# Kernel tuning notes

Hardware: AMD Instinct MI355X
Metric: run time of the kernel (lower is better)

## Reference

```python
import jax, jax.numpy as jnp
import numpy as np

H, KV, D, S = 32, 8, 128, 2048
HID = H * D
L = S  # cache length
LAYER_IDX = 0


def rotate_half(x, axis):
    x1, x2 = jnp.split(x, 2, axis=axis)
    return jnp.concatenate([-x2, x1], axis=axis)


def setup_inputs() -> dict:
    key = jax.random.key(0)
    ks = jax.random.split(key, 9)
    scale = 0.02
    hidden_states = jax.random.normal(ks[0], (1, HID, 1, S), jnp.float32)
    wq = jax.random.normal(ks[1], (H * D, HID), jnp.float32) * scale
    wk = jax.random.normal(ks[2], (KV * D, HID), jnp.float32) * scale
    wv = jax.random.normal(ks[3], (KV * D, HID), jnp.float32) * scale
    wo = jax.random.normal(ks[4], (HID, H * D), jnp.float32) * scale
    bq = jax.random.normal(ks[5], (H * D,), jnp.float32) * scale
    bk = jax.random.normal(ks[6], (KV * D,), jnp.float32) * scale
    bv = jax.random.normal(ks[7], (KV * D,), jnp.float32) * scale
    # RoPE tables (rotate-half convention): (1,1,S,D) and transposed (1,1,D,S)
    inv_freq = 1.0 / (10000.0 ** (np.arange(0, D, 2, dtype=np.float32) / D))
    t = np.arange(S, dtype=np.float32)
    freqs = np.outer(t, inv_freq)                    # (S, D/2)
    emb = np.concatenate([freqs, freqs], axis=-1)    # (S, D)
    cos = jnp.asarray(np.cos(emb), jnp.float32)[None, None]
    sin = jnp.asarray(np.sin(emb), jnp.float32)[None, None]
    cos_t = jnp.swapaxes(cos, -1, -2)
    sin_t = jnp.swapaxes(sin, -1, -2)
    # causal mask in transposed (cache_len, q_len) layout: key pos l visible iff l <= s
    lpos = np.arange(L)[:, None]
    spos = np.arange(S)[None, :]
    attention_mask = jnp.asarray(np.where(lpos <= spos, 0.0, -1e9).astype(np.float32))[None, None]
    key_cache = jnp.zeros((1, KV, L, D), jnp.float32)
    value_cache = jnp.zeros((1, KV, L, D), jnp.float32)
    return dict(hidden_states=hidden_states, wq=wq, bq=bq, wk=wk, bk=bk, wv=wv, bv=bv,
                wo=wo, cos=cos, sin=sin, cos_t=cos_t, sin_t=sin_t,
                attention_mask=attention_mask, key_cache=key_cache,
                value_cache=value_cache, cache_position=0)


def reference(hidden_states, wq, bq, wk, bk, wv, bv, wo, cos, sin, cos_t, sin_t,
              attention_mask, key_cache, value_cache, cache_position):
    x = hidden_states[0, :, 0, :]                          # (HID, S) channels-first
    q = wq @ x + bq[:, None]                               # (H*D, S)
    k = wk @ x + bk[:, None]                               # (KV*D, S)
    v = wv @ x + bv[:, None]
    q = q.reshape(H, D, S)                                 # (H, D, S)
    k = jnp.swapaxes(k.reshape(KV, D, S), 1, 2)            # (KV, S, D)
    v = jnp.swapaxes(v.reshape(KV, D, S), 1, 2)            # (KV, S, D)
    # RoPE: Q rotated along D (dim=-2 in NCHW), K along last dim
    q = q * cos_t[0] + rotate_half(q, axis=1) * sin_t[0]
    k = k * cos[0] + rotate_half(k, axis=2) * sin[0]
    # KV-cache in-place update at cache_position
    kc = jax.lax.dynamic_update_slice(key_cache, k[None], (LAYER_IDX, 0, cache_position, 0))
    vc = jax.lax.dynamic_update_slice(value_cache, v[None], (LAYER_IDX, 0, cache_position, 0))
    kk = kc[LAYER_IDX]                                     # (KV, L, D)
    vv = vc[LAYER_IDX]                                     # (KV, L, D)
    G = H // KV
    qg = q.reshape(KV, G, D, S)                            # group queries per KV head
    scores = jnp.einsum('kld,kgds->kgls', kk, qg) / jnp.sqrt(jnp.float32(D))
    scores = scores + attention_mask[0]                    # (1,L,S) broadcasts over (KV,G,L,S)
    w = jax.nn.softmax(scores, axis=2)                     # softmax over cache_len
    out = jnp.einsum('kgls,kld->kgsd', w, vv)              # (KV, G, S, D)
    out = jnp.swapaxes(out.reshape(H, S, D), 1, 2).reshape(H * D, S)
    y = wo @ out                                           # (HID, S)
    return y[None, :, None, :]                             # (1, HID, 1, S)
```

## Files before the change

kernel.cpp:

```cpp
#include <hip/hip_runtime.h>
#include <hip/hip_bf16.h>

#define H_   32
#define KV_  8
#define D_   128
#define S_   2048
#define HID_ 4096

typedef __attribute__((ext_vector_type(8))) short short8;
typedef short8 short8a __attribute__((may_alias));
typedef __attribute__((ext_vector_type(4))) float f32x4;
typedef unsigned short u16;
typedef unsigned int u32;

__device__ __forceinline__ u16 f2bf(float f) {
  union { float f; unsigned u; } a; a.f = f;
  unsigned r = a.u + 0x7fffu + ((a.u >> 16) & 1u);
  return (u16)(r >> 16);
}
__device__ __forceinline__ float bf2f(u16 h) {
  union { unsigned u; float f; } a; a.u = ((unsigned)h) << 16;
  return a.f;
}

#define GLOAD16(g, l) __builtin_amdgcn_global_load_lds( \
    (const __attribute__((address_space(1))) void*)(g), \
    (__attribute__((address_space(3))) void*)(l), 16, 0, 0)

__global__ void cast4_kernel(const float* __restrict__ s0, const float* __restrict__ s1,
                             const float* __restrict__ s2, const float* __restrict__ s3,
                             u16* __restrict__ d0, u16* __restrict__ d1,
                             u16* __restrict__ d2, u16* __restrict__ d3,
                             int n0, int n1, int n2, int n3) {
  int total = n0 + n1 + n2 + n3;
  for (int i = blockIdx.x * blockDim.x + threadIdx.x; i < total; i += gridDim.x * blockDim.x) {
    const float* s; u16* d; int k = i;
    if (k < n0) { s = s0; d = d0; }
    else if ((k -= n0) < n1) { s = s1; d = d1; }
    else if ((k -= n1) < n2) { s = s2; d = d2; }
    else { k -= n2; s = s3; d = d3; }
    float4 v = ((const float4*)s)[k];
    ushort4 o;
    o.x = f2bf(v.x); o.y = f2bf(v.y); o.z = f2bf(v.z); o.w = f2bf(v.w);
    ((ushort4*)d)[k] = o;
  }
}

__global__ __launch_bounds__(256) void transpose_cast_kernel(const float* __restrict__ in,
                                                             u16* __restrict__ out) {
  __shared__ float t[32][33];
  int tx = threadIdx.x & 31, ty = threadIdx.x >> 5;
  int s0 = blockIdx.x * 32, c0 = blockIdx.y * 32;
  #pragma unroll
  for (int i = 0; i < 4; i++)
    t[ty + i * 8][tx] = in[(size_t)(c0 + ty + i * 8) * S_ + s0 + tx];
  __syncthreads();
  #pragma unroll
  for (int i = 0; i < 4; i++)
    out[(size_t)(s0 + ty + i * 8) * HID_ + c0 + tx] = f2bf(t[tx][ty + i * 8]);
}

__device__ __forceinline__ short8 ldsfrag(const u16* base, int row, int ks, int kg) {
  int cb = (ks * 64 + kg * 16) ^ ((row & 7) << 4);
  return *(const short8a*)((const char*)base + row * 128 + cb);
}

template<int BM>
__global__ __launch_bounds__(512, 2) void gemm_t(const u16* __restrict__ A, const u16* __restrict__ Bt,
    const float* __restrict__ bq, const float* __restrict__ bk, const float* __restrict__ bv,
    u16* __restrict__ Cb, float* __restrict__ Cf, int M, int N, int K) {
  constexpr int CA = BM / 64;
  constexpr int CB = 4;
  constexpr int CA1 = (CA + 1) / 2;
  constexpr int MI = BM / 64;
  __shared__ alignas(16) u16 Asl[2][BM * 64];
  __shared__ alignas(16) u16 Bsl[2][256 * 64];
  int tid = threadIdx.x, wid = tid >> 6, lane = tid & 63;
  int lr = lane & 15, kg = lane >> 4;
  int gx = gridDim.x, nwg = gx * gridDim.y;
  int lid = blockIdx.y * gx + blockIdx.x;
  int q = nwg >> 3, r = nwg & 7;
  int xcd = lid & 7, idx = lid >> 3;
  int swz = (xcd < r ? xcd * (q + 1) : r * (q + 1) + (xcd - r) * q) + idx;
  int m0 = (swz / gx) * BM, n0 = (swz % gx) * 256;
  const u16* Ap = A + (size_t)m0 * K;
  const u16* Bp = Bt + (size_t)n0 * K;
  int wm = wid >> 2;
  int wn = wid & 3;
  f32x4 acc[2][2][MI][2] = {};
  int NT = K >> 6;

  auto STAGEC = [&](const u16* gp, int tile, int chunk, u16* base) {
    int p = tid * 16;
    int row = (chunk << 6) + (p >> 7);
    int gcb = (p & 127) ^ ((row & 7) << 4);
    const char* src = (const char*)gp + ((size_t)row * K + (tile << 6)) * 2 + gcb;
    char* dst = (char*)base + (chunk << 13) + (wid << 10);
    GLOAD16(src, dst);
  };
  auto LDA = [&](short8 (&af)[MI][2], const u16* base, int qm) {
    #pragma unroll
    for (int mi = 0; mi < MI; mi++)
      #pragma unroll
      for (int ks = 0; ks < 2; ks++)
        af[mi][ks] = ldsfrag(base, wm * (BM / 2) + qm * (BM / 4) + mi * 16 + lr, ks, kg);
  };
  auto LDB = [&](short8 (&bf)[2][2], const u16* base, int qn) {
    #pragma unroll
    for (int ni = 0; ni < 2; ni++)
      #pragma unroll
      for (int ks = 0; ks < 2; ks++)
        bf[ni][ks] = ldsfrag(base, wn * 64 + qn * 32 + ni * 16 + lr, ks, kg);
  };
  auto MM = [&](f32x4 (&a)[MI][2], short8 (&af)[MI][2], short8 (&bf)[2][2]) {
    __builtin_amdgcn_s_setprio(1);
    #pragma unroll
    for (int ks = 0; ks < 2; ks++)
      #pragma unroll
      for (int mi = 0; mi < MI; mi++)
        #pragma unroll
        for (int ni = 0; ni < 2; ni++)
          a[mi][ni] = __builtin_amdgcn_mfma_f32_16x16x32_bf16(af[mi][ks], bf[ni][ks], a[mi][ni], 0, 0, 0);
    __builtin_amdgcn_s_setprio(0);
  };
  #define BAR() __builtin_amdgcn_s_barrier()
  #define SB()  __builtin_amdgcn_sched_barrier(0)
  #define VMCNT(n) asm volatile("s_waitcnt vmcnt(" #n ")" ::: "memory")

  short8 af[MI][2], bfA[2][2], bfB[2][2];

  #pragma unroll
  for (int c = 0; c < CA; c++) STAGEC(Ap, 0, c, &Asl[0][0]);
  #pragma unroll
  for (int c = 0; c < CB; c++) STAGEC(Bp, 0, c, &Bsl[0][0]);
  #pragma unroll
  for (int c = 0; c < CB; c++) STAGEC(Bp, 1, c, &Bsl[1][0]);
  VMCNT(4);
  BAR();

  for (int T = 0; T < NT; T++) {
    int par = T & 1;
    u16* aC = &Asl[par][0];
    u16* bC = &Bsl[par][0];
    u16* aN = &Asl[par ^ 1][0];
    int tA = T + 1 < NT ? T + 1 : NT - 1;
    int tB = T + 2 < NT ? T + 2 : NT - 1;
    LDA(af, aC, 0); LDB(bfA, bC, 0);
    #pragma unroll
    for (int c = 0; c < CA1; c++) STAGEC(Ap, tA, c, aN);
    SB(); BAR();
    MM(acc[0][0], af, bfA);
    BAR();
    LDB(bfB, bC, 1);
    #pragma unroll
    for (int c = CA1; c < CA; c++) STAGEC(Ap, tA, c, aN);
    SB(); BAR();
    MM(acc[0][1], af, bfB);
    BAR();
    LDA(af, aC, 1);
    STAGEC(Bp, tB, 0, bC); STAGEC(Bp, tB, 1, bC);
    SB(); BAR();
    MM(acc[1][0], af, bfA);
    BAR();
    STAGEC(Bp, tB, 2, bC); STAGEC(Bp, tB, 3, bC);
    VMCNT(4);
    SB(); BAR();
    MM(acc[1][1], af, bfB);
    BAR();
  }
  #undef BAR
  #undef SB
  #undef VMCNT

  #pragma unroll
  for (int qm = 0; qm < 2; qm++)
    #pragma unroll
    for (int qn = 0; qn < 2; qn++)
      #pragma unroll
      for (int mi = 0; mi < MI; mi++)
        #pragma unroll
        for (int ni = 0; ni < 2; ni++) {
          int col = n0 + wn * 64 + qn * 32 + ni * 16 + lr;
          int rbase = m0 + wm * (BM / 2) + qm * (BM / 4) + mi * 16 + kg * 4;
          #pragma unroll
          for (int rr = 0; rr < 4; rr++) {
            int row = rbase + rr;
            float v = acc[qm][qn][mi][ni][rr];
            if (bq) v += row < 4096 ? bq[row] : (row < 5120 ? bk[row - 4096] : bv[row - 5120]);
            if (Cf) Cf[(size_t)row * N + col] = v;
            else    Cb[(size_t)row * N + col] = f2bf(v);
          }
        }
}

__global__ __launch_bounds__(256) void rope_transpose_kernel(const u16* __restrict__ in,
                                                             u16* __restrict__ out,
                                                             const float* __restrict__ cp,
                                                             const float* __restrict__ sp,
                                                             float oscale) {
  __shared__ u16 t[128][33];
  int h = blockIdx.x;
  int s0 = blockIdx.y * 32;
  int tid = threadIdx.x;
  #pragma unroll
  for (int i = 0; i < 16; i++) {
    int idx = tid + i * 256;
    int row = idx >> 5, sc = idx & 31;
    t[row][sc] = in[(size_t)(h * 128 + row) * S_ + s0 + sc];
  }
  __syncthreads();
  int d = tid & 127, sh = tid >> 7;
  int dl = d & 63;
  bool hi = d >= 64;
  #pragma unroll
  for (int j = 0; j < 16; j++) {
    int sl = sh * 16 + j;
    int s = s0 + sl;
    float x = bf2f(t[d][sl]);
    float p = bf2f(t[d ^ 64][sl]);
    float c  = cp[(size_t)s * D_ + dl];
    float sn = sp[(size_t)s * D_ + dl];
    float o = hi ? fmaf(p, sn, x * c) : fmaf(-p, sn, x * c);
    out[((size_t)h * S_ + s) * D_ + d] = f2bf(o * oscale);
  }
}

__global__ __launch_bounds__(256) void attn_v2(const u16* __restrict__ Q, const u16* __restrict__ K,
                                               const u16* __restrict__ V, u16* __restrict__ Ot) {
  __shared__ alignas(16) u16 Ks[2][64 * 128];
  __shared__ alignas(16) u16 Vs[2][128 * 64];
  __shared__ alignas(16) u16 Pl[4][2][16 * 64];
  int h = blockIdx.x;
  int qtile = (int)(gridDim.y - 1) - (int)blockIdx.y;
  int kv = h >> 2;
  int tid = threadIdx.x, wid = tid >> 6, lane = tid & 63;
  int lr = lane & 15, kg = lane >> 4;
  int q0w = qtile * 128 + wid * 32;
  const u16* Qb = Q + ((size_t)h * S_ + q0w) * D_;
  const u16* Kb = K + (size_t)kv * S_ * D_;
  const u16* Vb = V + (size_t)kv * D_ * S_;
  int sw = (lr & 7) << 3;

  short8 qf[2][4];
  #pragma unroll
  for (int m = 0; m < 2; m++)
    #pragma unroll
    for (int kk = 0; kk < 4; kk++)
      qf[m][kk] = *(const short8a*)(Qb + (size_t)(m * 16 + lr) * D_ + kk * 32 + kg * 8);

  f32x4 acc[2][8] = {};
  float mreg[2] = {-1e30f, -1e30f};
  float lsum[2] = {0.f, 0.f};

  int krow[4], kcb[4], vrow[4], vcb[4];
  #pragma unroll
  for (int j = 0; j < 4; j++) {
    int c = wid * 4 + j;
    int o = c * 1024 + lane * 16;
    krow[j] = o >> 8;
    kcb[j] = (o & 255) ^ ((krow[j] & 7) << 4);
    vrow[j] = o >> 7;
    vcb[j] = (o & 127) ^ ((vrow[j] & 7) << 4);
  }

  int nlt = 2 * qtile + 2;
  #pragma unroll
  for (int j = 0; j < 4; j++) {
    int c = wid * 4 + j;
    GLOAD16((const char*)Kb + ((size_t)krow[j] * D_) * 2 + kcb[j], (char*)Ks[0] + c * 1024);
    GLOAD16((const char*)Vb + ((size_t)vrow[j] * S_) * 2 + vcb[j], (char*)Vs[0] + c * 1024);
  }
  int cur = 0;
  for (int t = 0; t < nlt; t++) {
    __syncthreads();
    if (t + 1 < nlt) {
      int l1 = (t + 1) * 64;
      #pragma unroll
      for (int j = 0; j < 4; j++) {
        int c = wid * 4 + j;
        GLOAD16((const char*)Kb + ((size_t)(l1 + krow[j]) * D_) * 2 + kcb[j],
                (char*)Ks[cur ^ 1] + c * 1024);
        GLOAD16((const char*)Vb + ((size_t)vrow[j] * S_ + l1) * 2 + vcb[j],
                (char*)Vs[cur ^ 1] + c * 1024);
      }
    }
    int l0 = t * 64;
    bool act0 = l0 <= q0w + 15;
    bool act1 = l0 <= q0w + 31;
    if (act1) {
      const u16* Kc = Ks[cur];
      const u16* Vc = Vs[cur];
      f32x4 st[2][4] = {};
      #pragma unroll
      for (int ls = 0; ls < 4; ls++) {
        short8 kf[4];
        #pragma unroll
        for (int kk = 0; kk < 4; kk++)
          kf[kk] = *(const short8a*)&Kc[(ls * 16 + lr) * 128 + ((kk * 32 + kg * 8) ^ sw)];
        #pragma unroll
        for (int kk = 0; kk < 4; kk++) {
          st[0][ls] = __builtin_amdgcn_mfma_f32_16x16x32_bf16(kf[kk], qf[0][kk], st[0][ls], 0, 0, 0);
          st[1][ls] = __builtin_amdgcn_mfma_f32_16x16x32_bf16(kf[kk], qf[1][kk], st[1][ls], 0, 0, 0);
        }
      }
      #pragma unroll
      for (int m = 0; m < 2; m++) {
        bool act = m ? act1 : act0;
        if (!act) continue;
        int qrow = q0w + m * 16 + lr;
        if (l0 + 63 > q0w + m * 16) {
          #pragma unroll
          for (int ls = 0; ls < 4; ls++)
            #pragma unroll
            for (int rr = 0; rr < 4; rr++) {
              int l = l0 + ls * 16 + kg * 4 + rr;
              st[m][ls][rr] = (l <= qrow) ? st[m][ls][rr] : -1e30f;
            }
        }
        float rmax;
        {
          float a0 = fmaxf(fmaxf(st[m][0][0], st[m][0][1]), fmaxf(st[m][0][2], st[m][0][3]));
          float a1 = fmaxf(fmaxf(st[m][1][0], st[m][1][1]), fmaxf(st[m][1][2], st[m][1][3]));
          float a2 = fmaxf(fmaxf(st[m][2][0], st[m][2][1]), fmaxf(st[m][2][2], st[m][2][3]));
          float a3 = fmaxf(fmaxf(st[m][3][0], st[m][3][1]), fmaxf(st[m][3][2], st[m][3][3]));
          rmax = fmaxf(fmaxf(a0, a1), fmaxf(a2, a3));
        }
        rmax = fmaxf(rmax, __shfl_xor(rmax, 16, 64));
        rmax = fmaxf(rmax, __shfl_xor(rmax, 32, 64));
        if (__any(rmax > mreg[m] + 8.0f)) {
          float nm = fmaxf(mreg[m], rmax);
          float f = __builtin_amdgcn_exp2f(mreg[m] - nm);
          mreg[m] = nm;
          lsum[m] *= f;
          float fr0 = __shfl(f, kg * 4 + 0, 64);
          float fr1 = __shfl(f, kg * 4 + 1, 64);
          float fr2 = __shfl(f, kg * 4 + 2, 64);
          float fr3 = __shfl(f, kg * 4 + 3, 64);
          #pragma unroll
          for (int dc = 0; dc < 8; dc++) {
            acc[m][dc][0] *= fr0; acc[m][dc][1] *= fr1;
            acc[m][dc][2] *= fr2; acc[m][dc][3] *= fr3;
          }
        }
        float e[4][4];
        #pragma unroll
        for (int ls = 0; ls < 4; ls++)
          #pragma unroll
          for (int rr = 0; rr < 4; rr++)
            e[ls][rr] = __builtin_amdgcn_exp2f(st[m][ls][rr] - mreg[m]);
        float rs = 0.f;
        #pragma unroll
        for (int ls = 0; ls < 4; ls++)
          rs += (e[ls][0] + e[ls][1]) + (e[ls][2] + e[ls][3]);
        rs += __shfl_xor(rs, 16, 64);
        rs += __shfl_xor(rs, 32, 64);
        lsum[m] += rs;
        u16* Pw = &Pl[wid][m][0];
        #pragma unroll
        for (int ls = 0; ls < 4; ls++) {
          __hip_bfloat162 p01 = __float22bfloat162_rn(float2{e[ls][0], e[ls][1]});
          __hip_bfloat162 p23 = __float22bfloat162_rn(float2{e[ls][2], e[ls][3]});
          uint2 pk;
          pk.x = *(u32*)&p01;
          pk.y = *(u32*)&p23;
          *(uint2*)&Pw[lr * 64 + ((ls * 16 + kg * 4) ^ sw)] = pk;
        }
      }
      #pragma unroll
      for (int kk = 0; kk < 2; kk++) {
        short8 pf0 = {}, pf1;
        if (act0) pf0 = *(const short8a*)&Pl[wid][0][lr * 64 + ((kk * 32 + kg * 8) ^ sw)];
        pf1 = *(const short8a*)&Pl[wid][1][lr * 64 + ((kk * 32 + kg * 8) ^ sw)];
        #pragma unroll
        for (int dc = 0; dc < 8; dc++) {
          short8 vf = *(const short8a*)&Vc[(dc * 16 + lr) * 64 + ((kk * 32 + kg * 8) ^ sw)];
          if (act0) acc[0][dc] = __builtin_amdgcn_mfma_f32_16x16x32_bf16(pf0, vf, acc[0][dc], 0, 0, 0);
          acc[1][dc] = __builtin_amdgcn_mfma_f32_16x16x32_bf16(pf1, vf, acc[1][dc], 0, 0, 0);
        }
      }
    }
    cur ^= 1;
  }
  #pragma unroll
  for (int m = 0; m < 2; m++) {
    float inv0 = 1.0f / __shfl(lsum[m], kg * 4 + 0, 64);
    float inv1 = 1.0f / __shfl(lsum[m], kg * 4 + 1, 64);
    float inv2 = 1.0f / __shfl(lsum[m], kg * 4 + 2, 64);
    float inv3 = 1.0f / __shfl(lsum[m], kg * 4 + 3, 64);
    #pragma unroll
    for (int dc = 0; dc < 8; dc++) {
      int col = h * D_ + dc * 16 + lr;
      int qg = q0w + m * 16 + kg * 4;
      Ot[(size_t)(qg + 0) * HID_ + col] = f2bf(acc[m][dc][0] * inv0);
      Ot[(size_t)(qg + 1) * HID_ + col] = f2bf(acc[m][dc][1] * inv1);
      Ot[(size_t)(qg + 2) * HID_ + col] = f2bf(acc[m][dc][2] * inv2);
      Ot[(size_t)(qg + 3) * HID_ + col] = f2bf(acc[m][dc][3] * inv3);
    }
  }
}

static constexpr size_t OFF_WQKV = 0;
static constexpr size_t OFF_WO   = 50331648;
static constexpr size_t OFF_XT   = 83886080;
static constexpr size_t OFF_QKVC = 100663296;

#define QSCALE 0.1275176329533421f

extern "C" void kernel_launch(void* const* d_in, const int* in_sizes, int n_in,
                              void* d_out, int out_size, void* d_ws, size_t ws_size,
                              hipStream_t stream) {
  const float* x    = (const float*)d_in[0];
  const float* wq   = (const float*)d_in[1];
  const float* bq   = (const float*)d_in[2];
  const float* wk   = (const float*)d_in[3];
  const float* bk   = (const float*)d_in[4];
  const float* wv   = (const float*)d_in[5];
  const float* bv   = (const float*)d_in[6];
  const float* wo   = (const float*)d_in[7];
  const float* cosP = (const float*)d_in[8];
  const float* sinP = (const float*)d_in[9];
  char* ws = (char*)d_ws;
  u16* WQKV = (u16*)(ws + OFF_WQKV);
  u16* WO   = (u16*)(ws + OFF_WO);
  u16* XT   = (u16*)(ws + OFF_XT);
  u16* QKVC = (u16*)(ws + OFF_QKVC);
  u16* QT   = QKVC;
  u16* KT   = QKVC + (size_t)4096 * S_;
  u16* VB   = QKVC + (size_t)5120 * S_;
  u16* QATT = (u16*)(ws + 0);
  u16* KATT = (u16*)(ws + 16777216);
  u16* OT   = (u16*)(ws + 20971520);
  float* y = (float*)d_out;

  cast4_kernel<<<2048, 256, 0, stream>>>(
      wq, wk, wv, wo,
      WQKV, WQKV + (size_t)4096 * HID_, WQKV + (size_t)5120 * HID_, WO,
      (HID_ * HID_) / 4, (KV_ * D_ * HID_) / 4, (KV_ * D_ * HID_) / 4, (HID_ * HID_) / 4);
  transpose_cast_kernel<<<dim3(S_ / 32, HID_ / 32), 256, 0, stream>>>(x, XT);
  gemm_t<192><<<dim3(S_ / 256, 6144 / 192), 512, 0, stream>>>(WQKV, XT, bq, bk, bv,
                                                              QKVC, nullptr, 6144, S_, HID_);
  rope_transpose_kernel<<<dim3(H_, S_ / 32), 256, 0, stream>>>(QT, QATT, cosP, sinP, QSCALE);
  rope_transpose_kernel<<<dim3(KV_, S_ / 32), 256, 0, stream>>>(KT, KATT, cosP, sinP, 1.0f);
  attn_v2<<<dim3(H_, S_ / 128), 256, 0, stream>>>(QATT, KATT, VB, OT);
  gemm_t<128><<<dim3(S_ / 256, HID_ / 128), 512, 0, stream>>>(WO, OT, nullptr, nullptr, nullptr,
                                                              nullptr, y, HID_, S_, HID_);
}
```

Before: 382.0 us.

## Prefetch LDS fragments in QKV GEMM and split-K the output projection

Adds a PF variant of the GEMM that double-buffers A/B register fragments, loading the next tile's fragments before the last MFMA block so LDS reads overlap compute. The QKV projection uses it. The output projection switches to a 256-row tile with split-K over two partial outputs (one written into the reused XT workspace region), followed by a separate reduce-add kernel. This trades extra register pressure and an extra full read/write pass over the output against better LDS latency hiding and a different wave count for the output GEMM.

```diff
diff --git a/kernel.cpp b/kernel.cpp
--- a/kernel.cpp
+++ b/kernel.cpp
@@ -60,17 +60,28 @@
     out[(size_t)(s0 + ty + i * 8) * HID_ + c0 + tx] = f2bf(t[tx][ty + i * 8]);
 }
 
+__global__ void reduce_add_kernel(float* __restrict__ y, const float* __restrict__ p, int n4) {
+  int i = blockIdx.x * blockDim.x + threadIdx.x;
+  int st = gridDim.x * blockDim.x;
+  for (; i < n4; i += st) {
+    float4 a = ((const float4*)y)[i];
+    float4 b = ((const float4*)p)[i];
+    a.x += b.x; a.y += b.y; a.z += b.z; a.w += b.w;
+    ((float4*)y)[i] = a;
+  }
+}
+
 __device__ __forceinline__ short8 ldsfrag(const u16* base, int row, int ks, int kg) {
   int cb = (ks * 64 + kg * 16) ^ ((row & 7) << 4);
   return *(const short8a*)((const char*)base + row * 128 + cb);
 }
 
-template<int BM>
+template<int BM, bool PF>
 __global__ __launch_bounds__(512, 2) void gemm_t(const u16* __restrict__ A, const u16* __restrict__ Bt,
     const float* __restrict__ bq, const float* __restrict__ bk, const float* __restrict__ bv,
-    u16* __restrict__ Cb, float* __restrict__ Cf, int M, int N, int K) {
+    u16* __restrict__ Cb, float* __restrict__ Cf0, float* __restrict__ Cf1,
+    int N, int K, int kPerSplit) {
   constexpr int CA = BM / 64;
-  constexpr int CB = 4;
   constexpr int CA1 = (CA + 1) / 2;
   constexpr int MI = BM / 64;
   __shared__ alignas(16) u16 Asl[2][BM * 64];
@@ -83,12 +94,13 @@
   int xcd = lid & 7, idx = lid >> 3;
   int swz = (xcd < r ? xcd * (q + 1) : r * (q + 1) + (xcd - r) * q) + idx;
   int m0 = (swz / gx) * BM, n0 = (swz % gx) * 256;
-  const u16* Ap = A + (size_t)m0 * K;
-  const u16* Bp = Bt + (size_t)n0 * K;
-  int wm = wid >> 2;
-  int wn = wid & 3;
+  int k0 = blockIdx.z * kPerSplit;
+  int NT = kPerSplit >> 6;
+  float* Cf = blockIdx.z ? Cf1 : Cf0;
+  const u16* Ap = A + (size_t)m0 * K + k0;
+  const u16* Bp = Bt + (size_t)n0 * K + k0;
+  int wm = wid >> 2, wn = wid & 3;
   f32x4 acc[2][2][MI][2] = {};
-  int NT = K >> 6;
 
   auto STAGEC = [&](const u16* gp, int tile, int chunk, u16* base) {
     int p = tid * 16;
@@ -127,46 +139,79 @@
   #define SB()  __builtin_amdgcn_sched_barrier(0)
   #define VMCNT(n) asm volatile("s_waitcnt vmcnt(" #n ")" ::: "memory")
 
-  short8 af[MI][2], bfA[2][2], bfB[2][2];
-
   #pragma unroll
   for (int c = 0; c < CA; c++) STAGEC(Ap, 0, c, &Asl[0][0]);
   #pragma unroll
-  for (int c = 0; c < CB; c++) STAGEC(Bp, 0, c, &Bsl[0][0]);
-  #pragma unroll
-  for (int c = 0; c < CB; c++) STAGEC(Bp, 1, c, &Bsl[1][0]);
+  for (int c = 0; c < 4; c++) STAGEC(Bp, 0, c, &Bsl[0][0]);
+  #pragma unroll
+  for (int c = 0; c < 4; c++) STAGEC(Bp, 1, c, &Bsl[1][0]);
   VMCNT(4);
   BAR();
 
-  for (int T = 0; T < NT; T++) {
-    int par = T & 1;
-    u16* aC = &Asl[par][0];
-    u16* bC = &Bsl[par][0];
-    u16* aN = &Asl[par ^ 1][0];
-    int tA = T + 1 < NT ? T + 1 : NT - 1;
-    int tB = T + 2 < NT ? T + 2 : NT - 1;
-    LDA(af, aC, 0); LDB(bfA, bC, 0);
-    #pragma unroll
-    for (int c = 0; c < CA1; c++) STAGEC(Ap, tA, c, aN);
-    SB(); BAR();
-    MM(acc[0][0], af, bfA);
-    BAR();
-    LDB(bfB, bC, 1);
-    #pragma unroll
-    for (int c = CA1; c < CA; c++) STAGEC(Ap, tA, c, aN);
-    SB(); BAR();
-    MM(acc[0][1], af, bfB);
-    BAR();
-    LDA(af, aC, 1);
-    STAGEC(Bp, tB, 0, bC); STAGEC(Bp, tB, 1, bC);
-    SB(); BAR();
-    MM(acc[1][0], af, bfA);
-    BAR();
-    STAGEC(Bp, tB, 2, bC); STAGEC(Bp, tB, 3, bC);
-    VMCNT(4);
-    SB(); BAR();
-    MM(acc[1][1], af, bfB);
-    BAR();
+  if constexpr (PF) {
+    short8 afA[MI][2], afB[MI][2], bfA[2][2], bfB[2][2];
+    SB();
+    LDA(afA, &Asl[0][0], 0); LDB(bfA, &Bsl[0][0], 0);
+    for (int T = 0; T < NT; T++) {
+      int par = T & 1;
+      u16* aC = &Asl[par][0];     u16* bC = &Bsl[par][0];
+      u16* aN = &Asl[par ^ 1][0]; u16* bN = &Bsl[par ^ 1][0];
+      int tA = T + 1 < NT ? T + 1 : NT - 1;
+      int tB = T + 2 < NT ? T + 2 : NT - 1;
+      #pragma unroll
+      for (int c = 0; c < CA1; c++) STAGEC(Ap, tA, c, aN);
+      SB(); BAR(); SB();
+      LDB(bfB, bC, 1); LDA(afB, aC, 1);
+      MM(acc[0][0], afA, bfA);
+      BAR();
+      #pragma unroll
+      for (int c = CA1; c < CA; c++) STAGEC(Ap, tA, c, aN);
+      SB(); BAR();
+      MM(acc[0][1], afA, bfB);
+      BAR();
+      STAGEC(Bp, tB, 0, bC); STAGEC(Bp, tB, 1, bC);
+      SB(); BAR();
+      MM(acc[1][0], afB, bfA);
+      BAR();
+      STAGEC(Bp, tB, 2, bC); STAGEC(Bp, tB, 3, bC);
+      VMCNT(4);
+      SB(); BAR(); SB();
+      LDA(afA, aN, 0); LDB(bfA, bN, 0);
+      MM(acc[1][1], afB, bfB);
+      BAR();
+    }
+  } else {
+    short8 af[MI][2], bfA[2][2], bfB[2][2];
+    for (int T = 0; T < NT; T++) {
+      int par = T & 1;
+      u16* aC = &Asl[par][0];
+      u16* bC = &Bsl[par][0];
+      u16* aN = &Asl[par ^ 1][0];
+      int tA = T + 1 < NT ? T + 1 : NT - 1;
+      int tB = T + 2 < NT ? T + 2 : NT - 1;
+      LDA(af, aC, 0); LDB(bfA, bC, 0);
+      #pragma unroll
+      for (int c = 0; c < CA1; c++) STAGEC(Ap, tA, c, aN);
+      SB(); BAR();
+      MM(acc[0][0], af, bfA);
+      BAR();
+      LDB(bfB, bC, 1);
+      #pragma unroll
+      for (int c = CA1; c < CA; c++) STAGEC(Ap, tA, c, aN);
+      SB(); BAR();
+      MM(acc[0][1], af, bfB);
+      BAR();
+      LDA(af, aC, 1);
+      STAGEC(Bp, tB, 0, bC); STAGEC(Bp, tB, 1, bC);
+      SB(); BAR();
+      MM(acc[1][0], af, bfA);
+      BAR();
+      STAGEC(Bp, tB, 2, bC); STAGEC(Bp, tB, 3, bC);
+      VMCNT(4);
+      SB(); BAR();
+      MM(acc[1][1], af, bfB);
+      BAR();
+    }
   }
   #undef BAR
   #undef SB
@@ -430,6 +475,7 @@
   u16* QATT = (u16*)(ws + 0);
   u16* KATT = (u16*)(ws + 16777216);
   u16* OT   = (u16*)(ws + 20971520);
+  float* P1 = (float*)(ws + OFF_XT);
   float* y = (float*)d_out;
 
   cast4_kernel<<<2048, 256, 0, stream>>>(
@@ -437,11 +483,12 @@
       WQKV, WQKV + (size_t)4096 * HID_, WQKV + (size_t)5120 * HID_, WO,
       (HID_ * HID_) / 4, (KV_ * D_ * HID_) / 4, (KV_ * D_ * HID_) / 4, (HID_ * HID_) / 4);
   transpose_cast_kernel<<<dim3(S_ / 32, HID_ / 32), 256, 0, stream>>>(x, XT);
-  gemm_t<192><<<dim3(S_ / 256, 6144 / 192), 512, 0, stream>>>(WQKV, XT, bq, bk, bv,
-                                                              QKVC, nullptr, 6144, S_, HID_);
+  gemm_t<192, true><<<dim3(S_ / 256, 6144 / 192, 1), 512, 0, stream>>>(
+      WQKV, XT, bq, bk, bv, QKVC, nullptr, nullptr, S_, HID_, HID_);
   rope_transpose_kernel<<<dim3(H_, S_ / 32), 256, 0, stream>>>(QT, QATT, cosP, sinP, QSCALE);
   rope_transpose_kernel<<<dim3(KV_, S_ / 32), 256, 0, stream>>>(KT, KATT, cosP, sinP, 1.0f);
   attn_v2<<<dim3(H_, S_ / 128), 256, 0, stream>>>(QATT, KATT, VB, OT);
-  gemm_t<128><<<dim3(S_ / 256, HID_ / 128), 512, 0, stream>>>(WO, OT, nullptr, nullptr, nullptr,
-                                                              nullptr, y, HID_, S_, HID_);
-}
+  gemm_t<256, false><<<dim3(S_ / 256, HID_ / 256, 2), 512, 0, stream>>>(
+      WO, OT, nullptr, nullptr, nullptr, nullptr, y, P1, S_, HID_, HID_ / 2);
+  reduce_add_kernel<<<2048, 256, 0, stream>>>(y, P1, (HID_ * S_) / 4);
+}
```

After: 392.5 us. 2.7% more time.
